# Kernel tuning notes

Hardware: AMD Instinct MI355X
Metric: run time of the kernel (lower is better)

The kernel has to match this reference:

```python
import jax, jax.numpy as jnp
import numpy as np

B, N1, N2, D, E = 8, 1024, 256, 16, 16


def setup_inputs() -> dict:
    key = jax.random.key(0)
    ks = jax.random.split(key, 11)
    stdv = 1.0 / np.sqrt(E)
    u = lambda k, shape: jax.random.uniform(k, shape, jnp.float32, -stdv, stdv)
    inputs = jax.random.normal(ks[0], (B, N1, N2, D), dtype=jnp.float32)
    # adjacency matrices (dense, nonnegative); scaled for numerical sanity
    adj0 = jax.random.uniform(ks[1], (N1, N1), dtype=jnp.float32) / np.float32(np.sqrt(N1))
    adj1 = jax.random.uniform(ks[2], (N2, N2), dtype=jnp.float32) / np.float32(np.sqrt(N2))
    return {
        "inputs": inputs, "adj0": adj0, "adj1": adj1,
        "W": u(ks[3], (D, E)), "b": u(ks[4], (E,)),
        "W_s0": u(ks[5], (D, E)), "b_s0": u(ks[6], (E,)),
        "W_s1": u(ks[7], (D, E)), "b_s1": u(ks[8], (E,)),
        "W_s01": u(ks[9], (D, E)), "b_s01": u(ks[10], (E,)),
    }


def _helper(x, adj_modes, W, b):
    # TGCNHelper: mode-wise adjacency products along the given tensor modes,
    # then a linear projection on the feature axis.
    h = x
    for mode, A in adj_modes:
        if mode == 0:
            h = jnp.einsum('bijd,ik->bkjd', h, A)  # mode-0 (n1) aggregation
        else:
            h = jnp.einsum('bijd,jk->bikd', h, A)  # mode-1 (n2) aggregation
    return jnp.einsum('bijd,de->bije', h, W) + b


def reference(inputs, adj0, adj1, W, b, W_s0, b_s0, W_s1, b_s1, W_s01, b_s01):
    # dense mode-product branch: inputs x_{-1} W + bias
    h_lin = jnp.einsum('bijd,de->bije', inputs, W) + b
    # subsets of valid_modes [0,1]: {0}, {1}, {0,1}
    h0 = _helper(inputs, [(0, adj0)], W_s0, b_s0)
    h1 = _helper(inputs, [(1, adj1)], W_s1, b_s1)
    h01 = _helper(inputs, [(0, adj0), (1, adj1)], W_s01, b_s01)
    # stack + sum over last dim == direct sum; then ReLU
    return jax.nn.relu(h_lin + h0 + h1 + h01)
```

## Files before the change

kernel.cpp:

```cpp
#include <hip/hip_runtime.h>

#define BB  8
#define NN1 1024
#define NN2 256
#define DD  16
#define EE  16
#define NCOL (NN2 * DD)
#define SLPB 2

using bf16x8  = __attribute__((ext_vector_type(8))) short;
using f32x4   = __attribute__((ext_vector_type(4))) float;
using ushort8 = __attribute__((ext_vector_type(8))) unsigned short;

__device__ __forceinline__ ushort f2bf(float x) {
  unsigned u = __float_as_uint(x);
  unsigned r = (u + 0x7FFFu + ((u >> 16) & 1u)) >> 16;
  return (ushort)r;
}
__device__ __forceinline__ float bf2f(ushort u) {
  return __uint_as_float((unsigned)u << 16);
}
__device__ __forceinline__ unsigned pkbf(float a, float b) {
  return (unsigned)f2bf(a) | ((unsigned)f2bf(b) << 16);
}

#define GLDS16(g, l)                                                       \
  __builtin_amdgcn_global_load_lds(                                        \
      (const __attribute__((address_space(1))) void*)(g),                  \
      (__attribute__((address_space(3))) void*)(l), 16, 0, 0)

__global__ __launch_bounds__(256)
void k_prep(const float* __restrict__ src, ushort* __restrict__ dst,
            int nr, int kd, size_t srcBatch, size_t dstBatch) {
  __shared__ float tile[64][65];
  const int t = threadIdx.x;
  const int r0 = blockIdx.x * 64;
  const int k0 = blockIdx.y * 64;
  const float* s = src + (size_t)blockIdx.z * srcBatch;
  ushort* d = dst + (size_t)blockIdx.z * dstBatch;

#pragma unroll
  for (int it = 0; it < 4; ++it) {
    const int kr = it * 16 + (t >> 4);
    const int rc = (t & 15) * 4;
    float4 v = *reinterpret_cast<const float4*>(&s[(size_t)(k0 + kr) * nr + r0 + rc]);
    tile[kr][rc] = v.x; tile[kr][rc + 1] = v.y;
    tile[kr][rc + 2] = v.z; tile[kr][rc + 3] = v.w;
  }
  __syncthreads();

#pragma unroll
  for (int pass = 0; pass < 2; ++pass) {
    const int task = t + pass * 256;
    const int pr = task >> 3;
    const int gl = task & 7;
    const int r = r0 + pr;
    const int f = (r >> 1) & 3;
    const int klb = (gl >> 2) * 32 + ((gl & 3) ^ f) * 8;
    unsigned w[4];
#pragma unroll
    for (int e2 = 0; e2 < 4; ++e2)
      w[e2] = pkbf(tile[klb + e2 * 2][pr], tile[klb + e2 * 2 + 1][pr]);
    *reinterpret_cast<uint4*>(&d[(size_t)r * kd + k0 + gl * 8]) =
        *reinterpret_cast<const uint4*>(w);
  }
}

__global__ __launch_bounds__(256)
void k_mode0_mfma(const ushort* __restrict__ At, const ushort* __restrict__ Xt,
                  ushort* __restrict__ Y) {
  __shared__ ushort As[2][4096];
  __shared__ ushort Bs[2][4096];

  const int t = threadIdx.x;
  const int lane = t & 63;
  const int wid = t >> 6;
  const int wm = wid >> 1, wn = wid & 1;
  const int b  = blockIdx.x >> 5;
  const int c0 = (blockIdx.x & 31) << 7;
  const int p0 = blockIdx.y << 7;

  const ushort* Bb = Xt + (size_t)b * (NCOL * 1024);

  f32x4 acc[4][4];
#pragma unroll
  for (int i = 0; i < 4; ++i)
#pragma unroll
    for (int j = 0; j < 4; ++j) acc[i][j] = (f32x4)0.f;

  const int srow = wid * 32 + (lane >> 2);
  const int schk = (lane & 3) * 8;
  const size_t aoff0 = (size_t)(p0 + srow) * 1024 + schk;
  const size_t boff0 = (size_t)(c0 + srow) * 1024 + schk;
  const int lw0 = (wid * 32) * 32;
  const int lw1 = (wid * 32 + 16) * 32;

  const int lm = lane & 15, g = lane >> 4;
  int aro[4], bro[4];
#pragma unroll
  for (int f = 0; f < 4; ++f) {
    const int ra = wm * 64 + f * 16 + lm;
    aro[f] = ra * 32 + ((g ^ ((ra >> 1) & 3)) << 3);
    const int rw = wn * 64 + f * 16 + lm;
    bro[f] = rw * 32 + ((g ^ ((rw >> 1) & 3)) << 3);
  }

#define STAGE0(buf, kk)                                                    \
  do {                                                                     \
    GLDS16(At + aoff0 + (kk), &As[buf][lw0]);                              \
    GLDS16(At + aoff0 + 16 * 1024 + (kk), &As[buf][lw1]);                  \
    GLDS16(Bb + boff0 + (kk), &Bs[buf][lw0]);                              \
    GLDS16(Bb + boff0 + 16 * 1024 + (kk), &Bs[buf][lw1]);                  \
  } while (0)

  STAGE0(0, 0);
  int cur = 0;

  for (int k0 = 0; k0 < 1024; k0 += 32) {
    if (k0 + 32 < 1024) {
      STAGE0(cur ^ 1, k0 + 32);
      asm volatile("s_waitcnt vmcnt(4)" ::: "memory");
    } else {
      asm volatile("s_waitcnt vmcnt(0)" ::: "memory");
    }
    __builtin_amdgcn_s_barrier();
    __builtin_amdgcn_sched_barrier(0);

    bf16x8 af[4], bfr[4];
#pragma unroll
    for (int f = 0; f < 4; ++f)
      af[f] = *reinterpret_cast<const bf16x8*>(&As[cur][aro[f]]);
#pragma unroll
    for (int f = 0; f < 4; ++f)
      bfr[f] = *reinterpret_cast<const bf16x8*>(&Bs[cur][bro[f]]);

#pragma unroll
    for (int i = 0; i < 4; ++i)
#pragma unroll
      for (int j = 0; j < 4; ++j)
        acc[i][j] = __builtin_amdgcn_mfma_f32_16x16x32_bf16(af[i], bfr[j], acc[i][j], 0, 0, 0);

    __builtin_amdgcn_sched_barrier(0);
    __builtin_amdgcn_s_barrier();
    cur ^= 1;
  }
#undef STAGE0

  ushort* Yb = Y + (size_t)b * (NN1 * NCOL);
  const int orow = g * 4;
  const int ocol = lm;
#pragma unroll
  for (int i = 0; i < 4; ++i)
#pragma unroll
    for (int j = 0; j < 4; ++j) {
      const int p = p0 + wm * 64 + i * 16 + orow;
      const int c = c0 + wn * 64 + j * 16 + ocol;
      ushort* dst = Yb + (size_t)p * NCOL + c;
#pragma unroll
      for (int e = 0; e < 4; ++e) dst[(size_t)e * NCOL] = f2bf(acc[i][j][e]);
    }
}

__global__ __launch_bounds__(512)
void k_pm(const float* __restrict__ x, const ushort* __restrict__ y0,
          const ushort* __restrict__ A1t,
          const float* __restrict__ W,   const float* __restrict__ bW,
          const float* __restrict__ W0,  const float* __restrict__ b0,
          const float* __restrict__ W1,  const float* __restrict__ b1,
          const float* __restrict__ W01, const float* __restrict__ b01,
          float* __restrict__ out) {
  __shared__ ushort As[2][8192];
  __shared__ ushort St[8][SLPB * 16][32];

  const int t = threadIdx.x;
  const int lane = t & 63;
  const int wid = t >> 6;
  const int lm = lane & 15, g = lane >> 4;
  const int wq  = wid >> 1;
  const int wmi = wid & 1;
  const size_t sl0 = (size_t)blockIdx.x * SLPB;

  {
    const size_t base = (sl0 * NCOL) + (size_t)t * DD;
    const float4 x0 = *reinterpret_cast<const float4*>(&x[base]);
    const float4 x1 = *reinterpret_cast<const float4*>(&x[base + 4]);
    const float4 x2 = *reinterpret_cast<const float4*>(&x[base + 8]);
    const float4 x3 = *reinterpret_cast<const float4*>(&x[base + 12]);
    const uint4 yv0 = *reinterpret_cast<const uint4*>(&y0[base]);
    const uint4 yv1 = *reinterpret_cast<const uint4*>(&y0[base + 8]);
    unsigned xw0[4] = {pkbf(x0.x, x0.y), pkbf(x0.z, x0.w), pkbf(x1.x, x1.y), pkbf(x1.z, x1.w)};
    unsigned xw1[4] = {pkbf(x2.x, x2.y), pkbf(x2.z, x2.w), pkbf(x3.x, x3.y), pkbf(x3.z, x3.w)};
    *reinterpret_cast<uint4*>(&As[0][t * 16])     = *reinterpret_cast<const uint4*>(xw0);
    *reinterpret_cast<uint4*>(&As[0][t * 16 + 8]) = *reinterpret_cast<const uint4*>(xw1);
    *reinterpret_cast<uint4*>(&As[1][t * 16])     = yv0;
    *reinterpret_cast<uint4*>(&As[1][t * 16 + 8]) = yv1;
  }

  bf16x8 wfr, wfs;
#pragma unroll
  for (int jj = 0; jj < 8; ++jj) {
    const int k = g * 8 + jj;
    const float vr = (k < 16) ? W[k * 16 + lm]  : W0[(k - 16) * 16 + lm];
    const float vs = (k < 16) ? W1[k * 16 + lm] : W01[(k - 16) * 16 + lm];
    wfr[jj] = (short)f2bf(vr);
    wfs[jj] = (short)f2bf(vs);
  }
  const float bias = bW[lm] + b0[lm] + b1[lm] + b01[lm];

  __syncthreads();

  f32x4 acc[4];
#pragma unroll
  for (int i = 0; i < 4; ++i) {
    const int grp = wmi * 16 + wq * 4 + i;
    const int row = grp * 16 + lm;
    bf16x8 a;
    if (g < 2)
      a = *reinterpret_cast<const bf16x8*>(&As[0][row * 16 + g * 8]);
    else
      a = *reinterpret_cast<const bf16x8*>(&As[1][row * 16 + (g - 2) * 8]);

    f32x4 cb; cb[0] = bias; cb[1] = bias; cb[2] = bias; cb[3] = bias;
    acc[i] = __builtin_amdgcn_mfma_f32_16x16x32_bf16(a, wfr, cb, 0, 0, 0);
    const f32x4 sD = __builtin_amdgcn_mfma_f32_16x16x32_bf16(a, wfs, (f32x4)0.f, 0, 0, 0);

    const int m = wmi * 16 + lm;
    const int kc = wq * 2 + (i >> 1);
    const int chunkL = ((i & 1) << 1) + (g >> 1);
    const int phys = chunkL ^ ((m >> 1) & 3);
    unsigned pw[2] = {pkbf(sD[0], sD[1]), pkbf(sD[2], sD[3])};
    *reinterpret_cast<uint2*>(&St[kc][m][phys * 8 + (g & 1) * 4]) =
        *reinterpret_cast<const uint2*>(pw);
  }

  __syncthreads();

  const int srow = wid * 32 + (lane >> 2);
  const int schk = (lane & 3) * 8;

#define STAGEA(buf, kc)                                                    \
  do {                                                                     \
    GLDS16(A1t + (size_t)srow * 256 + (kc) * 32 + schk,                    \
           &As[buf][(wid * 32) * 32]);                                     \
    GLDS16(A1t + (size_t)(srow + 16) * 256 + (kc) * 32 + schk,             \
           &As[buf][(wid * 32 + 16) * 32]);                                \
  } while (0)

  int aro[4];
#pragma unroll
  for (int f = 0; f < 4; ++f) {
    const int ra = wq * 64 + f * 16 + lm;
    aro[f] = ra * 32 + ((g ^ ((ra >> 1) & 3)) << 3);
  }
  const int rwB = wmi * 16 + lm;
  const int bofs = (rwB * 32) + ((g ^ ((rwB >> 1) & 3)) << 3);

  STAGEA(0, 0);
  int cur = 0;
  for (int kc = 0; kc < 8; ++kc) {
    if (kc < 7) {
      STAGEA(cur ^ 1, kc + 1);
      asm volatile("s_waitcnt vmcnt(2)" ::: "memory");
    } else {
      asm volatile("s_waitcnt vmcnt(0)" ::: "memory");
    }
    __builtin_amdgcn_s_barrier();
    __builtin_amdgcn_sched_barrier(0);

    bf16x8 af[4];
#pragma unroll
    for (int f = 0; f < 4; ++f)
      af[f] = *reinterpret_cast<const bf16x8*>(&As[cur][aro[f]]);
    const bf16x8 bfr = *reinterpret_cast<const bf16x8*>(&St[kc][0][0] + bofs);

#pragma unroll
    for (int i = 0; i < 4; ++i)
      acc[i] = __builtin_amdgcn_mfma_f32_16x16x32_bf16(af[i], bfr, acc[i], 0, 0, 0);

    __builtin_amdgcn_sched_barrier(0);
    __builtin_amdgcn_s_barrier();
    cur ^= 1;
  }
#undef STAGEA

  float* os = out + (sl0 + wmi) * NCOL;
#pragma unroll
  for (int i = 0; i < 4; ++i) {
    const int qb = wq * 64 + i * 16 + g * 4;
#pragma unroll
    for (int rr = 0; rr < 4; ++rr)
      os[(size_t)(qb + rr) * EE + lm] = fmaxf(acc[i][rr], 0.f);
  }
}

extern "C" void kernel_launch(void* const* d_in, const int* in_sizes, int n_in,
                              void* d_out, int out_size, void* d_ws, size_t ws_size,
                              hipStream_t stream) {
  const float* x    = (const float*)d_in[0];
  const float* adj0 = (const float*)d_in[1];
  const float* adj1 = (const float*)d_in[2];
  const float* W    = (const float*)d_in[3];
  const float* bW   = (const float*)d_in[4];
  const float* Ws0  = (const float*)d_in[5];
  const float* bs0  = (const float*)d_in[6];
  const float* Ws1  = (const float*)d_in[7];
  const float* bs1  = (const float*)d_in[8];
  const float* Ws01 = (const float*)d_in[9];
  const float* bs01 = (const float*)d_in[10];
  float* out = (float*)d_out;

  const size_t SLICE = (size_t)NN1 * NCOL;
  const size_t AT_B  = (size_t)1024 * 1024 * 2;
  const size_t A1T_B = (size_t)256 * 256 * 2;
  const size_t XT_B  = (size_t)NCOL * 1024 * 2;
  const size_t Y0_B  = SLICE * 2;
  const size_t HEAD  = AT_B + A1T_B;
  const size_t PER_B = XT_B + Y0_B;

  int nb_max = (int)((ws_size > HEAD ? ws_size - HEAD : 0) / PER_B);
  if (nb_max > BB) nb_max = BB;
  if (nb_max < 1)  nb_max = 1;

  ushort* At  = (ushort*)d_ws;
  ushort* A1t = (ushort*)((char*)d_ws + AT_B);
  ushort* Xt  = (ushort*)((char*)d_ws + HEAD);
  ushort* y0  = (ushort*)((char*)d_ws + HEAD + (size_t)nb_max * XT_B);

  k_prep<<<dim3(16, 16, 1), 256, 0, stream>>>(adj0, At, 1024, 1024, 0, 0);
  k_prep<<<dim3(4, 4, 1), 256, 0, stream>>>(adj1, A1t, 256, 256, 0, 0);

  for (int c0 = 0; c0 < BB; c0 += nb_max) {
    const int nb = (BB - c0 < nb_max) ? (BB - c0) : nb_max;
    const float* xc = x   + (size_t)c0 * SLICE;
    float*       oc = out + (size_t)c0 * SLICE;

    k_prep<<<dim3(NCOL / 64, 16, nb), 256, 0, stream>>>(
        xc, Xt, NCOL, 1024, SLICE, (size_t)NCOL * 1024);

    dim3 g1(nb * 32, 8);
    k_mode0_mfma<<<g1, 256, 0, stream>>>(At, Xt, y0);

    dim3 g2(nb * NN1 / SLPB);
    k_pm<<<g2, 512, 0, stream>>>(xc, y0, A1t, W, bW, Ws0, bs0,
                                 Ws1, bs1, Ws01, bs01, oc);
  }
}
```

Baseline: 208.0 us.

## Enlarge mode-0 GEMM tiles to 256x256 with 8-wave phased pipeline and XCD remap

```diff
diff --git a/kernel.cpp b/kernel.cpp
--- a/kernel.cpp
+++ b/kernel.cpp
@@ -31,7 +31,7 @@
 
 __global__ __launch_bounds__(256)
 void k_prep(const float* __restrict__ src, ushort* __restrict__ dst,
-            int nr, int kd, size_t srcBatch, size_t dstBatch) {
+            int nr, int kd, size_t srcBatch, size_t dstBatch, int ps) {
   __shared__ float tile[64][65];
   const int t = threadIdx.x;
   const int r0 = blockIdx.x * 64;
@@ -55,8 +55,13 @@
     const int pr = task >> 3;
     const int gl = task & 7;
     const int r = r0 + pr;
-    const int f = (r >> 1) & 3;
-    const int klb = (gl >> 2) * 32 + ((gl & 3) ^ f) * 8;
+    int klb;
+    if (ps) {
+      klb = (gl ^ (r & 7)) * 8;
+    } else {
+      const int f = (r >> 1) & 3;
+      klb = (gl >> 2) * 32 + ((gl & 3) ^ f) * 8;
+    }
     unsigned w[4];
 #pragma unroll
     for (int e2 = 0; e2 < 4; ++e2)
@@ -66,95 +71,143 @@
   }
 }
 
-__global__ __launch_bounds__(256)
+__global__ __launch_bounds__(512, 1)
 void k_mode0_mfma(const ushort* __restrict__ At, const ushort* __restrict__ Xt,
                   ushort* __restrict__ Y) {
-  __shared__ ushort As[2][4096];
-  __shared__ ushort Bs[2][4096];
+  __shared__ ushort As[2][16384];
+  __shared__ ushort Bs[2][16384];
 
   const int t = threadIdx.x;
   const int lane = t & 63;
   const int wid = t >> 6;
-  const int wm = wid >> 1, wn = wid & 1;
-  const int b  = blockIdx.x >> 5;
-  const int c0 = (blockIdx.x & 31) << 7;
-  const int p0 = blockIdx.y << 7;
+  const int wm = wid >> 2;
+  const int wn = wid & 3;
+
+  const int nwg = (int)gridDim.x;
+  const int wg  = (int)blockIdx.x;
+  const int orig = (wg & 7) * (nwg >> 3) + (wg >> 3);
+  const int b  = orig >> 6;
+  const int rem = orig & 63;
+  const int c0 = (rem >> 2) << 8;
+  const int p0 = (rem & 3) << 8;
 
   const ushort* Bb = Xt + (size_t)b * (NCOL * 1024);
 
-  f32x4 acc[4][4];
-#pragma unroll
-  for (int i = 0; i < 4; ++i)
+  f32x4 acc[8][4];
+#pragma unroll
+  for (int i = 0; i < 8; ++i)
 #pragma unroll
     for (int j = 0; j < 4; ++j) acc[i][j] = (f32x4)0.f;
 
-  const int srow = wid * 32 + (lane >> 2);
-  const int schk = (lane & 3) * 8;
-  const size_t aoff0 = (size_t)(p0 + srow) * 1024 + schk;
-  const size_t boff0 = (size_t)(c0 + srow) * 1024 + schk;
-  const int lw0 = (wid * 32) * 32;
-  const int lw1 = (wid * 32 + 16) * 32;
-
   const int lm = lane & 15, g = lane >> 4;
-  int aro[4], bro[4];
+
+  int aoff2[8][2], boff2[4][2];
+#pragma unroll
+  for (int f = 0; f < 8; ++f) {
+    const int ra = wm * 128 + f * 16 + lm;
+#pragma unroll
+    for (int ks = 0; ks < 2; ++ks)
+      aoff2[f][ks] = ra * 64 + (((ks * 4 + g) ^ (ra & 7)) << 3);
+  }
 #pragma unroll
   for (int f = 0; f < 4; ++f) {
-    const int ra = wm * 64 + f * 16 + lm;
-    aro[f] = ra * 32 + ((g ^ ((ra >> 1) & 3)) << 3);
-    const int rw = wn * 64 + f * 16 + lm;
-    bro[f] = rw * 32 + ((g ^ ((rw >> 1) & 3)) << 3);
-  }
-
-#define STAGE0(buf, kk)                                                    \
-  do {                                                                     \
-    GLDS16(At + aoff0 + (kk), &As[buf][lw0]);                              \
-    GLDS16(At + aoff0 + 16 * 1024 + (kk), &As[buf][lw1]);                  \
-    GLDS16(Bb + boff0 + (kk), &Bs[buf][lw0]);                              \
-    GLDS16(Bb + boff0 + 16 * 1024 + (kk), &Bs[buf][lw1]);                  \
+    const int rb = wn * 64 + f * 16 + lm;
+#pragma unroll
+    for (int ks = 0; ks < 2; ++ks)
+      boff2[f][ks] = rb * 64 + (((ks * 4 + g) ^ (rb & 7)) << 3);
+  }
+
+#define STG_A(buf, kt, hA) do {                                            \
+    { const int r0_ = (hA) * 64 + wid * 8;                                 \
+      GLDS16(At + (size_t)(p0 + r0_ + (lane >> 3)) * 1024 + (kt) * 64 +    \
+                 (lane & 7) * 8, &As[buf][r0_ * 64]); }                    \
+    { const int r0_ = (hA) * 64 + 128 + wid * 8;                           \
+      GLDS16(At + (size_t)(p0 + r0_ + (lane >> 3)) * 1024 + (kt) * 64 +    \
+                 (lane & 7) * 8, &As[buf][r0_ * 64]); }                    \
   } while (0)
 
-  STAGE0(0, 0);
-  int cur = 0;
-
-  for (int k0 = 0; k0 < 1024; k0 += 32) {
-    if (k0 + 32 < 1024) {
-      STAGE0(cur ^ 1, k0 + 32);
-      asm volatile("s_waitcnt vmcnt(4)" ::: "memory");
+#define STG_B(buf, kt, hB) do {                                            \
+    { const int r0_ = (wid >> 2) * 64 + (hB) * 32 + (wid & 3) * 8;         \
+      GLDS16(Bb + (size_t)(c0 + r0_ + (lane >> 3)) * 1024 + (kt) * 64 +    \
+                 (lane & 7) * 8, &Bs[buf][r0_ * 64]); }                    \
+    { const int r0_ = (2 + (wid >> 2)) * 64 + (hB) * 32 + (wid & 3) * 8;   \
+      GLDS16(Bb + (size_t)(c0 + r0_ + (lane >> 3)) * 1024 + (kt) * 64 +    \
+                 (lane & 7) * 8, &Bs[buf][r0_ * 64]); }                    \
+  } while (0)
+
+#define VM6 asm volatile("s_waitcnt vmcnt(6)" ::: "memory")
+#define VM4 asm volatile("s_waitcnt vmcnt(4)" ::: "memory")
+#define VM2 asm volatile("s_waitcnt vmcnt(2)" ::: "memory")
+#define VM0 asm volatile("s_waitcnt vmcnt(0)" ::: "memory")
+#define NOWAIT ((void)0)
+#define NOSTG  ((void)0)
+
+#define PHASE(buf, qi, qj, STGSTMT, WAITSTMT) do {                         \
+    STGSTMT;                                                               \
+    WAITSTMT;                                                              \
+    __builtin_amdgcn_s_barrier();                                          \
+    __builtin_amdgcn_sched_barrier(0);                                     \
+    bf16x8 a_[4][2], b_[2][2];                                             \
+    _Pragma("unroll")                                                      \
+    for (int i_ = 0; i_ < 4; ++i_)                                         \
+      _Pragma("unroll")                                                    \
+      for (int ks_ = 0; ks_ < 2; ++ks_)                                    \
+        a_[i_][ks_] = *reinterpret_cast<const bf16x8*>(                    \
+            &As[buf][aoff2[(qi) * 4 + i_][ks_]]);                          \
+    _Pragma("unroll")                                                      \
+    for (int j_ = 0; j_ < 2; ++j_)                                         \
+      _Pragma("unroll")                                                    \
+      for (int ks_ = 0; ks_ < 2; ++ks_)                                    \
+        b_[j_][ks_] = *reinterpret_cast<const bf16x8*>(                    \
+            &Bs[buf][boff2[(qj) * 2 + j_][ks_]]);                          \
+    __builtin_amdgcn_s_setprio(1);                                         \
+    _Pragma("unroll")                                                      \
+    for (int ks_ = 0; ks_ < 2; ++ks_)                                      \
+      _Pragma("unroll")                                                    \
+      for (int i_ = 0; i_ < 4; ++i_)                                       \
+        _Pragma("unroll")                                                  \
+        for (int j_ = 0; j_ < 2; ++j_)                                     \
+          acc[(qi) * 4 + i_][(qj) * 2 + j_] =                              \
+              __builtin_amdgcn_mfma_f32_16x16x32_bf16(                     \
+                  a_[i_][ks_], b_[j_][ks_],                                \
+                  acc[(qi) * 4 + i_][(qj) * 2 + j_], 0, 0, 0);             \
+    __builtin_amdgcn_s_setprio(0);                                         \
+  } while (0)
+
+  STG_A(0, 0, 0); STG_B(0, 0, 0); STG_A(0, 0, 1); STG_B(0, 0, 1);
+
+  for (int it = 0; it < 8; ++it) {
+    const int t1 = 2 * it + 1, t2 = 2 * it + 2;
+    PHASE(0, 0, 0, STG_A(1, t1, 0), VM6);
+    PHASE(0, 1, 0, STG_B(1, t1, 0), VM6);
+    PHASE(0, 0, 1, STG_A(1, t1, 1), VM6);
+    PHASE(0, 1, 1, STG_B(1, t1, 1), VM6);
+    __builtin_amdgcn_s_barrier();
+    if (it < 7) {
+      PHASE(1, 0, 0, STG_A(0, t2, 0), VM6);
+      PHASE(1, 1, 0, STG_B(0, t2, 0), VM6);
+      PHASE(1, 0, 1, STG_A(0, t2, 1), VM6);
+      PHASE(1, 1, 1, STG_B(0, t2, 1), VM6);
     } else {
-      asm volatile("s_waitcnt vmcnt(0)" ::: "memory");
+      PHASE(1, 0, 0, NOSTG, VM4);
+      PHASE(1, 1, 0, NOSTG, VM2);
+      PHASE(1, 0, 1, NOSTG, VM0);
+      PHASE(1, 1, 1, NOSTG, NOWAIT);
     }
     __builtin_amdgcn_s_barrier();
-    __builtin_amdgcn_sched_barrier(0);
-
-    bf16x8 af[4], bfr[4];
-#pragma unroll
-    for (int f = 0; f < 4; ++f)
-      af[f] = *reinterpret_cast<const bf16x8*>(&As[cur][aro[f]]);
-#pragma unroll
-    for (int f = 0; f < 4; ++f)
-      bfr[f] = *reinterpret_cast<const bf16x8*>(&Bs[cur][bro[f]]);
-
-#pragma unroll
-    for (int i = 0; i < 4; ++i)
-#pragma unroll
-      for (int j = 0; j < 4; ++j)
-        acc[i][j] = __builtin_amdgcn_mfma_f32_16x16x32_bf16(af[i], bfr[j], acc[i][j], 0, 0, 0);
-
-    __builtin_amdgcn_sched_barrier(0);
-    __builtin_amdgcn_s_barrier();
-    cur ^= 1;
-  }
-#undef STAGE0
-
-  ushort* Yb = Y + (size_t)b * (NN1 * NCOL);
+  }
+#undef PHASE
+#undef STG_A
+#undef STG_B
+
+  ushort* Yb = Y + (size_t)b * ((size_t)NN1 * NCOL);
   const int orow = g * 4;
-  const int ocol = lm;
-#pragma unroll
-  for (int i = 0; i < 4; ++i)
+#pragma unroll
+  for (int i = 0; i < 8; ++i)
 #pragma unroll
     for (int j = 0; j < 4; ++j) {
-      const int p = p0 + wm * 64 + i * 16 + orow;
-      const int c = c0 + wn * 64 + j * 16 + ocol;
+      const int p = p0 + wm * 128 + i * 16 + orow;
+      const int c = c0 + wn * 64 + j * 16 + lm;
       ushort* dst = Yb + (size_t)p * NCOL + c;
 #pragma unroll
       for (int e = 0; e < 4; ++e) dst[(size_t)e * NCOL] = f2bf(acc[i][j][e]);
@@ -326,8 +379,8 @@
   ushort* Xt  = (ushort*)((char*)d_ws + HEAD);
   ushort* y0  = (ushort*)((char*)d_ws + HEAD + (size_t)nb_max * XT_B);
 
-  k_prep<<<dim3(16, 16, 1), 256, 0, stream>>>(adj0, At, 1024, 1024, 0, 0);
-  k_prep<<<dim3(4, 4, 1), 256, 0, stream>>>(adj1, A1t, 256, 256, 0, 0);
+  k_prep<<<dim3(16, 16, 1), 256, 0, stream>>>(adj0, At, 1024, 1024, 0, 0, 1);
+  k_prep<<<dim3(4, 4, 1), 256, 0, stream>>>(adj1, A1t, 256, 256, 0, 0, 0);
 
   for (int c0 = 0; c0 < BB; c0 += nb_max) {
     const int nb = (BB - c0 < nb_max) ? (BB - c0) : nb_max;
@@ -335,10 +388,10 @@
     float*       oc = out + (size_t)c0 * SLICE;
 
     k_prep<<<dim3(NCOL / 64, 16, nb), 256, 0, stream>>>(
-        xc, Xt, NCOL, 1024, SLICE, (size_t)NCOL * 1024);
-
-    dim3 g1(nb * 32, 8);
-    k_mode0_mfma<<<g1, 256, 0, stream>>>(At, Xt, y0);
+        xc, Xt, NCOL, 1024, SLICE, (size_t)NCOL * 1024, 1);
+
+    dim3 g1(nb * 64);
+    k_mode0_mfma<<<g1, 512, 0, stream>>>(At, Xt, y0);
 
     dim3 g2(nb * NN1 / SLPB);
     k_pm<<<g2, 512, 0, stream>>>(xc, y0, A1t, W, bW, Ws0, bs0,
```

Measured after the change: 373.7 us. 79.7% more time.
